# Optimization experiments

Measured on AMD Instinct MI355X. Metric: run time of the kernel, lower is better.

## Reference

```python
import jax, jax.numpy as jnp
import numpy as np

B, S, D, H = 4, 2048, 2048, 16
HD = D // H  # 128
ROPE_THETA = 10000.0


def apply_rope(x, pos, theta=ROPE_THETA):
    # x: [b, h, s, d], pos: [s] int. Interleaved-pair RoPE.
    d = x.shape[-1]
    inv_freq = theta ** (-jnp.arange(0, d, 2, dtype=jnp.float32) / d)  # [d/2]
    ang = pos.astype(jnp.float32)[:, None] * inv_freq[None, :]         # [s, d/2]
    cos, sin = jnp.cos(ang), jnp.sin(ang)
    x1, x2 = x[..., ::2], x[..., 1::2]                                  # [b,h,s,d/2]
    r1 = x1 * cos - x2 * sin
    r2 = x1 * sin + x2 * cos
    return jnp.stack([r1, r2], axis=-1).reshape(x.shape).astype(x.dtype)


def setup_inputs() -> dict:
    key = jax.random.key(0)
    kx, kq, kk, kv, ko = jax.random.split(key, 5)
    w_scale = 0.02
    return {
        "x": jax.random.normal(kx, (B, S, D), dtype=jnp.float32),
        "wq": jax.random.normal(kq, (D, D), dtype=jnp.float32) * w_scale,
        "wk": jax.random.normal(kk, (D, D), dtype=jnp.float32) * w_scale,
        "wv": jax.random.normal(kv, (D, D), dtype=jnp.float32) * w_scale,
        "wo": jax.random.normal(ko, (D, D), dtype=jnp.float32) * w_scale,
        "token_positions": jnp.arange(S, dtype=jnp.int32),
    }


def reference(x, wq, wk, wv, wo, token_positions):
    b, s, d = x.shape
    # QKV projections: weight layout is [d_out, d_in] (torch nn.Parameter convention)
    Q = jnp.einsum("bsd,kd->bsk", x, wq).reshape(b, s, H, HD).transpose(0, 2, 1, 3)
    K = jnp.einsum("bsd,kd->bsk", x, wk).reshape(b, s, H, HD).transpose(0, 2, 1, 3)
    V = jnp.einsum("bsd,kd->bsk", x, wv).reshape(b, s, H, HD).transpose(0, 2, 1, 3)
    Q = apply_rope(Q, token_positions)
    K = apply_rope(K, token_positions)
    # naive causal attention: full [b,h,s,s] score matrix
    scores = jnp.einsum("bhqd,bhkd->bhqk", Q, K) / jnp.sqrt(jnp.float32(HD))
    causal = jnp.tril(jnp.ones((s, s), dtype=bool))
    neg_inf = jnp.finfo(scores.dtype).min
    scores = jnp.where(causal[None, None], scores, neg_inf)
    probs = jax.nn.softmax(scores, axis=-1)
    O = jnp.einsum("bhqk,bhkd->bhqd", probs, V)
    O = O.transpose(0, 2, 1, 3).reshape(b, s, H * HD)
    return jnp.einsum("bsv,dv->bsd", O, wo)
```

## Files before the change

### kernel.cpp

```cpp
#include <hip/hip_runtime.h>
#include <cstdint>

typedef _Float16 f16;
typedef __attribute__((ext_vector_type(8))) _Float16 f16x8;
typedef __attribute__((ext_vector_type(4))) float f32x4;

constexpr int Bc  = 4;
constexpr int Sc  = 2048;
constexpr int Dc  = 2048;
constexpr int Hc  = 16;
constexpr int HDc = 128;

__global__ void cast_all_kernel(const float* __restrict__ x,  const float* __restrict__ wq,
                                const float* __restrict__ wk, const float* __restrict__ wv,
                                const float* __restrict__ wo,
                                f16* __restrict__ xh,  f16* __restrict__ wqh,
                                f16* __restrict__ wkh, f16* __restrict__ wvh,
                                f16* __restrict__ woh)
{
    long bid = blockIdx.x;
    const float* src; f16* dst; long off;
    if (bid < 8192)       { src = x;  dst = xh;  off = bid * 2048; }
    else {
        int r = (int)((bid - 8192) >> 11);
        off = ((bid - 8192) & 2047) * 2048;
        switch (r) {
            case 0:  src = wq; dst = wqh; break;
            case 1:  src = wk; dst = wkh; break;
            case 2:  src = wv; dst = wvh; break;
            default: src = wo; dst = woh; break;
        }
    }
    long i = off + (long)threadIdx.x * 8;
    float4 a = *(const float4*)(src + i);
    float4 b = *(const float4*)(src + i + 4);
    f16x8 o = { (f16)a.x, (f16)a.y, (f16)a.z, (f16)a.w,
                (f16)b.x, (f16)b.y, (f16)b.z, (f16)b.w };
    *(f16x8*)(dst + i) = o;
}

__device__ __forceinline__ void async_cp16(const f16* g, f16* l)
{
    __builtin_amdgcn_global_load_lds(
        (__attribute__((address_space(1))) void*)(g),
        (__attribute__((address_space(3))) void*)(l), 16, 0, 0);
}

template<typename OUT_T>
__global__ __launch_bounds__(512, 2) void gemm_bt8(
    const f16* __restrict__ A, const f16* __restrict__ W,
    OUT_T* __restrict__ C, int M, int N, int K)
{
    __shared__ alignas(16) f16 As[4][8192];
    __shared__ alignas(16) f16 Bs[4][8192];

    const int tid  = threadIdx.x;
    const int wave = tid >> 6, lane = tid & 63;
    const int l16  = lane & 15, quad = lane >> 4;
    const int wm   = wave >> 2, wn = wave & 3;

    const int nwg = (int)gridDim.x;
    int bid = (int)blockIdx.x;
    int wg  = ((nwg & 7) == 0) ? ((bid & 7) * (nwg >> 3) + (bid >> 3)) : bid;
    const int ntile = N >> 8;
    const int mt = wg / ntile, nt = wg % ntile;
    const int m0 = mt << 8, n0 = nt << 8;

    const int  prow = tid >> 2;
    const int  lch  = (((tid & 3) ^ ((prow >> 1) & 3)) << 3);
    const f16* Asrc = A + (long)(m0 + prow) * K + lch;
    const f16* Bsrc = W + (long)(n0 + prow) * K + lch;
    const long rsk  = (long)K << 7;
    const int  dst0 = wave << 9;

    const int nkt = K >> 5;

    auto stA = [&](int kt) {
        const f16* g = Asrc + ((long)kt << 5);
        int s = kt & 3;
        async_cp16(g,       &As[s][dst0]);
        async_cp16(g + rsk, &As[s][4096 + dst0]);
    };
    auto stB = [&](int kt) {
        const f16* g = Bsrc + ((long)kt << 5);
        int s = kt & 3;
        async_cp16(g,       &Bs[s][dst0]);
        async_cp16(g + rsk, &Bs[s][4096 + dst0]);
    };

    const int coff = ((quad ^ ((l16 >> 1) & 3)) << 3);
    const int arow = wm * 128 + l16;
    const int brow = wn * 64  + l16;

    f32x4 acc[8][4];
#pragma unroll
    for (int i = 0; i < 8; i++)
#pragma unroll
        for (int j = 0; j < 4; j++) acc[i][j] = (f32x4){0.f, 0.f, 0.f, 0.f};

    stA(0); stB(0);
    if (nkt > 1) {
        stA(1); stB(1);
        asm volatile("s_waitcnt vmcnt(4)" ::: "memory");
    } else {
        asm volatile("s_waitcnt vmcnt(0)" ::: "memory");
    }
    __builtin_amdgcn_s_barrier();
    __builtin_amdgcn_sched_barrier(0);

    for (int kt = 0; kt < nkt; ++kt) {
        const int s = kt & 3;
        const f16* as = &As[s][(long)arow * 32 + coff];
        const f16* bs = &Bs[s][(long)brow * 32 + coff];

        f16x8 bfr[4], afr[4];
#pragma unroll
        for (int j = 0; j < 4; ++j) bfr[j] = *(const f16x8*)(bs + j * 512);
#pragma unroll
        for (int i = 0; i < 4; ++i) afr[i] = *(const f16x8*)(as + i * 512);
        if (kt + 2 < nkt) stA(kt + 2);
        asm volatile("s_waitcnt lgkmcnt(0)" ::: "memory");
        __builtin_amdgcn_sched_barrier(0);
        __builtin_amdgcn_s_setprio(1);
#pragma unroll
        for (int i = 0; i < 4; ++i)
#pragma unroll
            for (int j = 0; j < 4; ++j)
                acc[i][j] = __builtin_amdgcn_mfma_f32_16x16x32_f16(afr[i], bfr[j], acc[i][j], 0, 0, 0);
        __builtin_amdgcn_s_setprio(0);

        f16x8 afr2[4];
#pragma unroll
        for (int i = 0; i < 4; ++i) afr2[i] = *(const f16x8*)(as + (i + 4) * 512);
        if (kt + 2 < nkt) stB(kt + 2);
        asm volatile("s_waitcnt lgkmcnt(0)" ::: "memory");
        __builtin_amdgcn_sched_barrier(0);
        __builtin_amdgcn_s_setprio(1);
#pragma unroll
        for (int i = 0; i < 4; ++i)
#pragma unroll
            for (int j = 0; j < 4; ++j)
                acc[i + 4][j] = __builtin_amdgcn_mfma_f32_16x16x32_f16(afr2[i], bfr[j], acc[i + 4][j], 0, 0, 0);
        __builtin_amdgcn_s_setprio(0);

        if (kt + 2 < nkt) asm volatile("s_waitcnt vmcnt(4)" ::: "memory");
        else              asm volatile("s_waitcnt vmcnt(0)" ::: "memory");
        __builtin_amdgcn_s_barrier();
        __builtin_amdgcn_sched_barrier(0);
    }

#pragma unroll
    for (int i = 0; i < 8; ++i) {
        int row = m0 + wm * 128 + i * 16 + quad * 4;
#pragma unroll
        for (int j = 0; j < 4; ++j) {
            int col = n0 + wn * 64 + j * 16 + l16;
#pragma unroll
            for (int r = 0; r < 4; ++r)
                C[(long)(row + r) * N + col] = (OUT_T)acc[i][j][r];
        }
    }
}

__global__ void rope_kernel(f16* __restrict__ Q, f16* __restrict__ K,
                            const int* __restrict__ pos, long npairs)
{
    long t = (long)blockIdx.x * blockDim.x + threadIdx.x;
    if (t >= 2 * npairs) return;
    f16* P = Q;
    long p = t;
    if (p >= npairs) { P = K; p -= npairs; }
    int  i    = (int)(p & 63);
    long rest = p >> 6;
    int  h    = (int)(rest & (Hc - 1));
    long row  = rest >> 4;
    int  s    = (int)(row & (Sc - 1));

    float inv = expf(-(float)i * (9.210340371976184f / 64.0f));
    float ang = (float)pos[s] * inv;
    float sn, cs;
    sincosf(ang, &sn, &cs);

    long idx = row * Dc + (long)h * HDc + 2 * i;
    unsigned int u = *(const unsigned int*)(P + idx);
    float x1 = (float)((const f16*)&u)[0];
    float x2 = (float)((const f16*)&u)[1];
    f16 o[2] = { (f16)(x1 * cs - x2 * sn), (f16)(x1 * sn + x2 * cs) };
    *(unsigned int*)(P + idx) = *(const unsigned int*)o;
}

__device__ __forceinline__ int swz(int row, int col, int ldshift) {
    return (row << ldshift) + (((((col >> 3) ^ ((row >> 1) & 7)) << 3) | (col & 7)));
}

__global__ __launch_bounds__(256, 2) void attn_kernel(
    const f16* __restrict__ Q, const f16* __restrict__ Kg,
    const f16* __restrict__ Vg, f16* __restrict__ O)
{
    __shared__ alignas(16) f16 Kt[64 * 128];
    __shared__ alignas(16) f16 Vt[128 * 64];
    __shared__ alignas(16) f16 Pl[128 * 64];

    const int tid  = threadIdx.x;
    const int wave = tid >> 6, lane = tid & 63;
    const int l16  = lane & 15, quad = lane >> 4;

    const int L  = (int)blockIdx.x;
    const int bh = (L & 7) + 8 * (L >> 7);
    const int qi = 15 - ((L >> 3) & 15);
    const int b  = bh >> 4, h = bh & 15;
    const long base = (long)b * Sc * Dc + (long)h * HDc;
    const float cexp = 0.12751742366f;

    long koff[4];
    f16* kdst[4];
#pragma unroll
    for (int j = 0; j < 4; j++) {
        int row_l = j * 16 + wave * 4 + (lane >> 4);
        int chg   = (lane & 15) ^ ((row_l >> 1) & 7);
        koff[j]   = base + (long)row_l * Dc + chg * 8;
        kdst[j]   = (f16*)&Kt[(j * 16 + wave * 4) * 128];
    }
    const int vd0 = lane * 2;

    f16x8 ones;
#pragma unroll
    for (int i = 0; i < 8; i++) ones[i] = (f16)1.0f;

    unsigned int vreg[2][8];
    auto load_v = [&](int k0) {
#pragma unroll
        for (int j = 0; j < 2; j++) {
            int kk0 = wave * 8 + j * 32;
#pragma unroll
            for (int i2 = 0; i2 < 8; i2++)
                vreg[j][i2] = *(const unsigned int*)&Vg[base + (long)(k0 + kk0 + i2) * Dc + vd0];
        }
    };
    auto load_k_async = [&](int k0) {
#pragma unroll
        for (int j = 0; j < 4; j++)
            async_cp16(Kg + koff[j] + (long)k0 * Dc, kdst[j]);
    };

    const int q0  = qi * 128;
    const int nkt = 2 * qi + 2;
    const int rlo = q0 + wave * 32;

    f16x8 qf[2][4];
#pragma unroll
    for (int im = 0; im < 2; im++)
#pragma unroll
        for (int kk = 0; kk < 4; kk++)
            qf[im][kk] = *(const f16x8*)&Q[base + (long)(q0 + wave * 32 + im * 16 + l16) * Dc
                                           + kk * 32 + quad * 8];

    f32x4 oacc[2][8];
    f32x4 lacc[2];
#pragma unroll
    for (int im = 0; im < 2; im++) {
        lacc[im] = (f32x4){0.f, 0.f, 0.f, 0.f};
#pragma unroll
        for (int nt = 0; nt < 8; nt++) oacc[im][nt] = (f32x4){0.f, 0.f, 0.f, 0.f};
    }

    load_k_async(0);
    load_v(0);
    for (int kt = 0; kt < nkt; kt++) {
        const int k0 = kt * 64;
        __syncthreads();
#pragma unroll
        for (int j = 0; j < 2; j++) {
            int kk0 = wave * 8 + j * 32;
            f16x8 lo, hi;
#pragma unroll
            for (int i2 = 0; i2 < 8; i2++) {
                lo[i2] = ((const f16*)&vreg[j][i2])[0];
                hi[i2] = ((const f16*)&vreg[j][i2])[1];
            }
            *(f16x8*)&Vt[swz(vd0,     kk0, 6)] = lo;
            *(f16x8*)&Vt[swz(vd0 + 1, kk0, 6)] = hi;
        }
        __syncthreads();

        const bool compute = (k0 <= rlo + 31);
        if (compute) {
            f32x4 sf[2][4];
#pragma unroll
            for (int im = 0; im < 2; im++)
#pragma unroll
                for (int in = 0; in < 4; in++) sf[im][in] = (f32x4){0.f, 0.f, 0.f, 0.f};
#pragma unroll
            for (int kk = 0; kk < 4; kk++) {
                f16x8 bf[4];
#pragma unroll
                for (int in = 0; in < 4; in++)
                    bf[in] = *(const f16x8*)&Kt[swz(in * 16 + l16, kk * 32 + quad * 8, 7)];
#pragma unroll
                for (int im = 0; im < 2; im++)
#pragma unroll
                    for (int in = 0; in < 4; in++)
                        sf[im][in] = __builtin_amdgcn_mfma_f32_16x16x32_f16(qf[im][kk], bf[in], sf[im][in], 0, 0, 0);
            }

#pragma unroll
            for (int im = 0; im < 2; im++) {
                const int rbase = rlo + im * 16;
                const bool need_mask = (k0 + 63 > rbase);
#pragma unroll
                for (int in = 0; in < 4; in++) {
#pragma unroll
                    for (int r = 0; r < 4; r++) {
                        float p = __builtin_amdgcn_exp2f(sf[im][in][r] * cexp);
                        if (need_mask) {
                            int kc  = k0 + in * 16 + l16;
                            int row = rbase + quad * 4 + r;
                            p = (kc <= row) ? p : 0.f;
                        }
                        Pl[swz(wave * 32 + im * 16 + quad * 4 + r, in * 16 + l16, 6)] = (f16)p;
                    }
                }
            }
        }
        __syncthreads();

        if (kt + 1 < nkt) {
            load_k_async(k0 + 64);
            load_v(k0 + 64);
        }

        if (compute) {
#pragma unroll
            for (int kk = 0; kk < 2; kk++) {
                f16x8 pf[2];
#pragma unroll
                for (int im = 0; im < 2; im++)
                    pf[im] = *(const f16x8*)&Pl[swz(wave * 32 + im * 16 + l16, kk * 32 + quad * 8, 6)];
#pragma unroll
                for (int im = 0; im < 2; im++)
                    lacc[im] = __builtin_amdgcn_mfma_f32_16x16x32_f16(pf[im], ones, lacc[im], 0, 0, 0);
#pragma unroll
                for (int nt = 0; nt < 8; nt++) {
                    f16x8 vf = *(const f16x8*)&Vt[swz(nt * 16 + l16, kk * 32 + quad * 8, 6)];
#pragma unroll
                    for (int im = 0; im < 2; im++)
                        oacc[im][nt] = __builtin_amdgcn_mfma_f32_16x16x32_f16(pf[im], vf, oacc[im][nt], 0, 0, 0);
                }
            }
        }
    }

#pragma unroll
    for (int im = 0; im < 2; im++) {
        int qrow = q0 + wave * 32 + im * 16 + quad * 4;
#pragma unroll
        for (int r = 0; r < 4; r++) {
            float inv = 1.0f / lacc[im][r];
#pragma unroll
            for (int nt = 0; nt < 8; nt++)
                O[base + (long)(qrow + r) * Dc + nt * 16 + l16] = (f16)(oacc[im][nt][r] * inv);
        }
    }
}

extern "C" void kernel_launch(void* const* d_in, const int* in_sizes, int n_in,
                              void* d_out, int out_size, void* d_ws, size_t ws_size,
                              hipStream_t stream)
{
    const float* x  = (const float*)d_in[0];
    const float* wq = (const float*)d_in[1];
    const float* wk = (const float*)d_in[2];
    const float* wv = (const float*)d_in[3];
    const float* wo = (const float*)d_in[4];
    const int*  pos = (const int*)d_in[5];
    float* out = (float*)d_out;

    const long E = (long)Bc * Sc * Dc;
    const long W = (long)Dc * Dc;
    f16* ws  = (f16*)d_ws;
    f16* xh  = ws;
    f16* wqh = ws + E;
    f16* wkh = wqh + W;
    f16* wvh = wkh + W;
    f16* woh = wvh + W;
    f16* Qh  = woh + W;
    f16* Kh  = Qh + E;
    f16* Vh  = Kh + E;
    f16* Oh  = xh;

    cast_all_kernel<<<dim3(16384), 256, 0, stream>>>(x, wq, wk, wv, wo,
                                                     xh, wqh, wkh, wvh, woh);

    dim3 gg((Bc * Sc / 256) * (Dc / 256));
    gemm_bt8<f16><<<gg, 512, 0, stream>>>(xh, wqh, Qh, Bc * Sc, Dc, Dc);
    gemm_bt8<f16><<<gg, 512, 0, stream>>>(xh, wkh, Kh, Bc * Sc, Dc, Dc);
    gemm_bt8<f16><<<gg, 512, 0, stream>>>(xh, wvh, Vh, Bc * Sc, Dc, Dc);

    long npairs = (long)Bc * Sc * Hc * (HDc / 2);
    rope_kernel<<<dim3(2 * npairs / 256), 256, 0, stream>>>(Qh, Kh, pos, npairs);

    attn_kernel<<<dim3(1024), 256, 0, stream>>>(Qh, Kh, Vh, Oh);

    gemm_bt8<float><<<gg, 512, 0, stream>>>(Oh, woh, out, Bc * Sc, Dc, Dc);
}
```

Before: 631.2 us.

## Fuse QKV projections into one GEMM with RoPE applied in the epilogue

Concatenates wq/wk/wv (already contiguous in the workspace) so a single GEMM with N=3*D writes an interleaved QKV buffer, and attention reads it with stride 3*D. RoPE is applied in the GEMM epilogue using a precomputed cos/sin table and a lane shuffle to fetch the pair partner, which removes the separate rope kernel's read-modify-write pass over Q and K. This also cuts three launches down to one with a larger grid. The cost is strided Q/K/V reads in attention and an extra table lookup in the epilogue.

```diff
diff --git a/kernel.cpp b/kernel.cpp
--- a/kernel.cpp
+++ b/kernel.cpp
@@ -10,6 +10,7 @@
 constexpr int Dc  = 2048;
 constexpr int Hc  = 16;
 constexpr int HDc = 128;
+constexpr int LDq = 3 * Dc;
 
 __global__ void cast_all_kernel(const float* __restrict__ x,  const float* __restrict__ wq,
                                 const float* __restrict__ wk, const float* __restrict__ wv,
@@ -39,6 +40,16 @@
     *(f16x8*)(dst + i) = o;
 }
 
+__global__ void gen_rope_tab(const int* __restrict__ pos, float2* __restrict__ tab)
+{
+    int s = blockIdx.x, i = threadIdx.x;
+    float inv = expf(-(float)i * (9.210340371976184f / 64.0f));
+    float ang = (float)pos[s] * inv;
+    float sn, cs;
+    sincosf(ang, &sn, &cs);
+    tab[s * 64 + i] = make_float2(cs, sn);
+}
+
 __device__ __forceinline__ void async_cp16(const f16* g, f16* l)
 {
     __builtin_amdgcn_global_load_lds(
@@ -46,10 +57,11 @@
         (__attribute__((address_space(3))) void*)(l), 16, 0, 0);
 }
 
-template<typename OUT_T>
+template<typename OUT_T, bool ROPE>
 __global__ __launch_bounds__(512, 2) void gemm_bt8(
     const f16* __restrict__ A, const f16* __restrict__ W,
-    OUT_T* __restrict__ C, int M, int N, int K)
+    OUT_T* __restrict__ C, const float2* __restrict__ tab,
+    int M, int N, int K)
 {
     __shared__ alignas(16) f16 As[4][8192];
     __shared__ alignas(16) f16 Bs[4][8192];
@@ -155,38 +167,25 @@
 #pragma unroll
         for (int j = 0; j < 4; ++j) {
             int col = n0 + wn * 64 + j * 16 + l16;
-#pragma unroll
-            for (int r = 0; r < 4; ++r)
-                C[(long)(row + r) * N + col] = (OUT_T)acc[i][j][r];
-        }
-    }
-}
-
-__global__ void rope_kernel(f16* __restrict__ Q, f16* __restrict__ K,
-                            const int* __restrict__ pos, long npairs)
-{
-    long t = (long)blockIdx.x * blockDim.x + threadIdx.x;
-    if (t >= 2 * npairs) return;
-    f16* P = Q;
-    long p = t;
-    if (p >= npairs) { P = K; p -= npairs; }
-    int  i    = (int)(p & 63);
-    long rest = p >> 6;
-    int  h    = (int)(rest & (Hc - 1));
-    long row  = rest >> 4;
-    int  s    = (int)(row & (Sc - 1));
-
-    float inv = expf(-(float)i * (9.210340371976184f / 64.0f));
-    float ang = (float)pos[s] * inv;
-    float sn, cs;
-    sincosf(ang, &sn, &cs);
-
-    long idx = row * Dc + (long)h * HDc + 2 * i;
-    unsigned int u = *(const unsigned int*)(P + idx);
-    float x1 = (float)((const f16*)&u)[0];
-    float x2 = (float)((const f16*)&u)[1];
-    f16 o[2] = { (f16)(x1 * cs - x2 * sn), (f16)(x1 * sn + x2 * cs) };
-    *(unsigned int*)(P + idx) = *(const unsigned int*)o;
+            if (ROPE && col < 4096) {
+                const int  ip = (col & 127) >> 1;
+                const bool ev = !(col & 1);
+#pragma unroll
+                for (int r = 0; r < 4; ++r) {
+                    float v = acc[i][j][r];
+                    float p = __shfl_xor(v, 1, 64);
+                    int   sfx = (row + r) & (Sc - 1);
+                    float2 cs = tab[sfx * 64 + ip];
+                    float o = ev ? (v * cs.x - p * cs.y) : (p * cs.y + v * cs.x);
+                    C[(long)(row + r) * N + col] = (OUT_T)o;
+                }
+            } else {
+#pragma unroll
+                for (int r = 0; r < 4; ++r)
+                    C[(long)(row + r) * N + col] = (OUT_T)acc[i][j][r];
+            }
+        }
+    }
 }
 
 __device__ __forceinline__ int swz(int row, int col, int ldshift) {
@@ -209,7 +208,8 @@
     const int bh = (L & 7) + 8 * (L >> 7);
     const int qi = 15 - ((L >> 3) & 15);
     const int b  = bh >> 4, h = bh & 15;
-    const long base = (long)b * Sc * Dc + (long)h * HDc;
+    const long bi = (long)b * Sc * LDq + (long)h * HDc;
+    const long bo = (long)b * Sc * Dc  + (long)h * HDc;
     const float cexp = 0.12751742366f;
 
     long koff[4];
@@ -218,7 +218,7 @@
     for (int j = 0; j < 4; j++) {
         int row_l = j * 16 + wave * 4 + (lane >> 4);
         int chg   = (lane & 15) ^ ((row_l >> 1) & 7);
-        koff[j]   = base + (long)row_l * Dc + chg * 8;
+        koff[j]   = bi + (long)row_l * LDq + chg * 8;
         kdst[j]   = (f16*)&Kt[(j * 16 + wave * 4) * 128];
     }
     const int vd0 = lane * 2;
@@ -234,13 +234,13 @@
             int kk0 = wave * 8 + j * 32;
 #pragma unroll
             for (int i2 = 0; i2 < 8; i2++)
-                vreg[j][i2] = *(const unsigned int*)&Vg[base + (long)(k0 + kk0 + i2) * Dc + vd0];
+                vreg[j][i2] = *(const unsigned int*)&Vg[bi + (long)(k0 + kk0 + i2) * LDq + vd0];
         }
     };
     auto load_k_async = [&](int k0) {
 #pragma unroll
         for (int j = 0; j < 4; j++)
-            async_cp16(Kg + koff[j] + (long)k0 * Dc, kdst[j]);
+            async_cp16(Kg + koff[j] + (long)k0 * LDq, kdst[j]);
     };
 
     const int q0  = qi * 128;
@@ -252,7 +252,7 @@
     for (int im = 0; im < 2; im++)
 #pragma unroll
         for (int kk = 0; kk < 4; kk++)
-            qf[im][kk] = *(const f16x8*)&Q[base + (long)(q0 + wave * 32 + im * 16 + l16) * Dc
+            qf[im][kk] = *(const f16x8*)&Q[bi + (long)(q0 + wave * 32 + im * 16 + l16) * LDq
                                            + kk * 32 + quad * 8];
 
     f32x4 oacc[2][8];
@@ -358,7 +358,7 @@
             float inv = 1.0f / lacc[im][r];
 #pragma unroll
             for (int nt = 0; nt < 8; nt++)
-                O[base + (long)(qrow + r) * Dc + nt * 16 + l16] = (f16)(oacc[im][nt][r] * inv);
+                O[bo + (long)(qrow + r) * Dc + nt * 16 + l16] = (f16)(oacc[im][nt][r] * inv);
         }
     }
 }
@@ -375,31 +375,30 @@
     const int*  pos = (const int*)d_in[5];
     float* out = (float*)d_out;
 
-    const long E = (long)Bc * Sc * Dc;
-    const long W = (long)Dc * Dc;
-    f16* ws  = (f16*)d_ws;
-    f16* xh  = ws;
-    f16* wqh = ws + E;
-    f16* wkh = wqh + W;
-    f16* wvh = wkh + W;
-    f16* woh = wvh + W;
-    f16* Qh  = woh + W;
-    f16* Kh  = Qh + E;
-    f16* Vh  = Kh + E;
-    f16* Oh  = xh;
+    const long E  = (long)Bc * Sc * Dc;
+    const long W  = (long)Dc * Dc;
+    const long EQ = (long)Bc * Sc * LDq;
+    f16* ws   = (f16*)d_ws;
+    f16* xh   = ws;
+    f16* wqh  = ws + E;
+    f16* wkh  = wqh + W;
+    f16* wvh  = wkh + W;
+    f16* woh  = wvh + W;
+    f16* QKV  = woh + W;
+    float2* tab = (float2*)(QKV + EQ);
+    f16* Oh   = xh;
 
     cast_all_kernel<<<dim3(16384), 256, 0, stream>>>(x, wq, wk, wv, wo,
                                                      xh, wqh, wkh, wvh, woh);
+    gen_rope_tab<<<dim3(Sc), 64, 0, stream>>>(pos, tab);
+
+    dim3 gq((Bc * Sc / 256) * (3 * Dc / 256));
+    gemm_bt8<f16, true><<<gq, 512, 0, stream>>>(xh, wqh, QKV, tab,
+                                                Bc * Sc, 3 * Dc, Dc);
+
+    attn_kernel<<<dim3(1024), 256, 0, stream>>>(QKV, QKV + Dc, QKV + 2 * Dc, Oh);
 
     dim3 gg((Bc * Sc / 256) * (Dc / 256));
-    gemm_bt8<f16><<<gg, 512, 0, stream>>>(xh, wqh, Qh, Bc * Sc, Dc, Dc);
-    gemm_bt8<f16><<<gg, 512, 0, stream>>>(xh, wkh, Kh, Bc * Sc, Dc, Dc);
-    gemm_bt8<f16><<<gg, 512, 0, stream>>>(xh, wvh, Vh, Bc * Sc, Dc, Dc);
-
-    long npairs = (long)Bc * Sc * Hc * (HDc / 2);
-    rope_kernel<<<dim3(2 * npairs / 256), 256, 0, stream>>>(Qh, Kh, pos, npairs);
-
-    attn_kernel<<<dim3(1024), 256, 0, stream>>>(Qh, Kh, Vh, Oh);
-
-    gemm_bt8<float><<<gg, 512, 0, stream>>>(Oh, woh, out, Bc * Sc, Dc, Dc);
-}
+    gemm_bt8<float, false><<<gg, 512, 0, stream>>>(Oh, woh, out, nullptr,
+                                                   Bc * Sc, Dc, Dc);
+}
```

Result: faster. 618.2 us (-2.1%).
